# Kernel tuning notes

Measured on AMD Instinct MI355X. Metric: run time of the kernel, lower is better.

Reference implementation:

```python
import jax, jax.numpy as jnp
import numpy as np

K = 16  # neighbors, incl. self


def setup_inputs() -> dict:
    key = jax.random.key(0)
    ks = jax.random.split(key, 16)
    N, C = 8192, 256  # points, channels (inter_channels == in_channels == C)
    s = 0.05
    inp = {
        'coords': jax.random.uniform(ks[0], (N, 3), dtype=jnp.float32) * 100.0,
        'feats': jax.random.normal(ks[1], (N, C), dtype=jnp.float32),
        'theta_w': jax.random.normal(ks[2], (C, C), dtype=jnp.float32) * s,
        'theta_b': jax.random.normal(ks[3], (C,), dtype=jnp.float32) * s,
        'phi_w': jax.random.normal(ks[4], (C, C), dtype=jnp.float32) * s,
        'phi_b': jax.random.normal(ks[5], (C,), dtype=jnp.float32) * s,
        'g_w': jax.random.normal(ks[6], (C, C), dtype=jnp.float32) * s,
        'g_b': jax.random.normal(ks[7], (C,), dtype=jnp.float32) * s,
        'pe1_w1': jax.random.normal(ks[8], (3, C), dtype=jnp.float32) * s,
        'pe1_b1': jax.random.normal(ks[9], (C,), dtype=jnp.float32) * s,
        'pe1_w2': jax.random.normal(ks[10], (C, C), dtype=jnp.float32) * s,
        'pe1_b2': jax.random.normal(ks[11], (C,), dtype=jnp.float32) * s,
        'W_w': jax.random.normal(ks[12], (C, C), dtype=jnp.float32) * s,
        'W_b': jax.random.normal(ks[13], (C,), dtype=jnp.float32) * s,
    }
    return inp


def reference(coords, feats, theta_w, theta_b, phi_w, phi_b, g_w, g_b,
              pe1_w1, pe1_b1, pe1_w2, pe1_b2, W_w, W_b):
    C = feats.shape[-1]
    # KNN (squared dists, includes self as nearest) == pytorch3d knn_points
    sq = jnp.sum(coords * coords, axis=-1)  # [N]
    d2 = sq[:, None] + sq[None, :] - 2.0 * (coords @ coords.T)  # [N,N]
    _, idx = jax.lax.top_k(-d2, K)  # [N,K] sorted by ascending distance

    nn_coords = coords[idx]            # [N,K,3] knn gather
    nn_feats = feats[idx]              # [N,K,C]

    theta_f = feats @ theta_w + theta_b          # [N,C]
    phi_f = nn_feats @ phi_w + phi_b             # [N,K,C]

    delta_coords = nn_coords - coords[:, None, :]  # [N,K,3]
    # pe1 MLP; NOTE: original code uses pe1 for both pe1 and pe2 (shared)
    pe = jax.nn.relu(delta_coords @ pe1_w1 + pe1_b1) @ pe1_w2 + pe1_b2  # [N,K,C]

    delta_features = (pe * (theta_f[:, None, :] - phi_f) + pe) / jnp.sqrt(jnp.float32(C))
    sim = jax.nn.softmax(delta_features, axis=1)  # softmax over K neighbors

    g_feats = nn_feats @ g_w + g_b               # [N,K,C]
    y = jnp.sum(sim * g_feats, axis=1)           # [N,C]

    # W (1x1 Minkowski conv == per-point linear) + residual
    return y @ W_w + W_b + feats
```

## Files before the change

kernel.cpp:

```cpp
#include <hip/hip_runtime.h>

typedef __bf16 bf16_t;
typedef bf16_t bf16x8 __attribute__((ext_vector_type(8)));
typedef bf16_t bf16x4 __attribute__((ext_vector_type(4)));
typedef bf16_t bf16x2 __attribute__((ext_vector_type(2)));
typedef float f32x4 __attribute__((ext_vector_type(4)));
typedef unsigned long long u64;

#define N_PTS 8192
#define C_DIM 256
#define K_NN 16

#define GRID_G    16
#define GRID_NC   (GRID_G * GRID_G * GRID_G)
#define GRID_CELL 6.25f
#define GRID_INV  0.16f

#define CAST_NBLK 2048
#define PREPW_NBLK 320
__global__ __launch_bounds__(256) void prep_kernel(
    const float* __restrict__ feats, bf16_t* __restrict__ fb,
    const float* __restrict__ w0, const float* __restrict__ w1,
    const float* __restrict__ w2, const float* __restrict__ w3,
    const float* __restrict__ w4, bf16_t* __restrict__ wt_base,
    int* __restrict__ cellCount, int* __restrict__ gcount) {
    const int b = blockIdx.x;
    const int t = threadIdx.x;

    if (b < CAST_NBLK) {
        int i = (b * 256 + t) * 4;
        float4 v = *(const float4*)(feats + i);
        bf16x4 o;
        o[0] = (bf16_t)v.x; o[1] = (bf16_t)v.y; o[2] = (bf16_t)v.z; o[3] = (bf16_t)v.w;
        *(bf16x4*)(fb + i) = o;
    } else if (b < CAST_NBLK + PREPW_NBLK) {
        int pb = b - CAST_NBLK;
        int m = pb >> 6;
        int bx = pb & 63;
        const float* src = (m == 0) ? w0 : (m == 1) ? w1 : (m == 2) ? w2 : (m == 3) ? w3 : w4;
        bf16_t* dst = wt_base + m * (C_DIM * C_DIM);
#pragma unroll
        for (int i = 0; i < 4; ++i) {
            int o = bx * 1024 + i * 256 + t;
            int tkb = o >> 9;
            int rem = o & 511;
            int lm = rem >> 5;
            int r = rem & 31;
            int k = (tkb & 7) * 32 + r;
            int n = (tkb >> 3) * 16 + lm;
            dst[o] = (bf16_t)src[k * C_DIM + n];
        }
    } else {
        int zb = b - CAST_NBLK - PREPW_NBLK;
        cellCount[zb * 256 + t] = 0;
        if (zb == 0 && t == 0) *gcount = 0;
    }
}

__global__ __launch_bounds__(256) void grid_count_kernel(const float* __restrict__ coords,
                                                         int* __restrict__ cellCount,
                                                         int* __restrict__ cid) {
    int i = blockIdx.x * 256 + threadIdx.x;
    float x = coords[3 * i + 0], y = coords[3 * i + 1], z = coords[3 * i + 2];
    int cx = (int)(x * GRID_INV); if (cx > GRID_G - 1) cx = GRID_G - 1;
    int cy = (int)(y * GRID_INV); if (cy > GRID_G - 1) cy = GRID_G - 1;
    int cz = (int)(z * GRID_INV); if (cz > GRID_G - 1) cz = GRID_G - 1;
    int c = (cx * GRID_G + cy) * GRID_G + cz;
    cid[i] = c;
    atomicAdd(&cellCount[c], 1);
}

__global__ __launch_bounds__(256) void grid_scan_kernel(const int* __restrict__ cellCount,
                                                        int* __restrict__ cellStart,
                                                        int* __restrict__ cellPtr) {
    __shared__ int part[256];
    int t = threadIdx.x;
    int base = t * 16;
    int v[16];
    int sum = 0;
#pragma unroll
    for (int i = 0; i < 16; ++i) { v[i] = cellCount[base + i]; sum += v[i]; }
    part[t] = sum;
    __syncthreads();
    for (int off = 1; off < 256; off <<= 1) {
        int x = (t >= off) ? part[t - off] : 0;
        __syncthreads();
        part[t] += x;
        __syncthreads();
    }
    int acc = part[t] - sum;
#pragma unroll
    for (int i = 0; i < 16; ++i) {
        cellStart[base + i] = acc;
        cellPtr[base + i] = acc;
        acc += v[i];
    }
    if (t == 255) cellStart[GRID_NC] = acc;
}

__global__ __launch_bounds__(256) void grid_scatter_kernel(
    const float* __restrict__ coords, const int* __restrict__ cid, int* __restrict__ cellPtr,
    float4* __restrict__ sp4, int* __restrict__ sidx) {
    int i = blockIdx.x * 256 + threadIdx.x;
    int c = cid[i];
    int pos = atomicAdd(&cellPtr[c], 1);
    float x = coords[3 * i + 0], y = coords[3 * i + 1], z = coords[3 * i + 2];
    float sq = __fadd_rn(__fadd_rn(__fmul_rn(x, x), __fmul_rn(y, y)), __fmul_rn(z, z));
    sp4[pos] = make_float4(x, y, z, sq);
    sidx[pos] = i;
}

__global__ __launch_bounds__(256) void knn_grid_kernel(
    const float* __restrict__ coords, const int* __restrict__ cellStart,
    const float4* __restrict__ sp4, const int* __restrict__ sidx,
    int* __restrict__ idx_out, int* __restrict__ glist, int* __restrict__ gcount) {
    const int tid = threadIdx.x;
    const int wave = tid >> 6, lane = tid & 63;
    const int q = blockIdx.x * 4 + wave;

    __shared__ int segBase[4][25];
    __shared__ int segPref[4][26];

    const float qx = coords[3 * q + 0], qy = coords[3 * q + 1], qz = coords[3 * q + 2];
    const float sqi = __fadd_rn(__fadd_rn(__fmul_rn(qx, qx), __fmul_rn(qy, qy)),
                                __fmul_rn(qz, qz));

    int cx = (int)(qx * GRID_INV); if (cx > GRID_G - 1) cx = GRID_G - 1;
    int cy = (int)(qy * GRID_INV); if (cy > GRID_G - 1) cy = GRID_G - 1;
    int cz = (int)(qz * GRID_INV); if (cz > GRID_G - 1) cz = GRID_G - 1;
    int wx0 = cx - 2; if (wx0 < 0) wx0 = 0;
    int wx1 = cx + 2; if (wx1 > GRID_G - 1) wx1 = GRID_G - 1;
    int wy0 = cy - 2; if (wy0 < 0) wy0 = 0;
    int wy1 = cy + 2; if (wy1 > GRID_G - 1) wy1 = GRID_G - 1;
    int wz0 = cz - 2; if (wz0 < 0) wz0 = 0;
    int wz1 = cz + 2; if (wz1 > GRID_G - 1) wz1 = GRID_G - 1;

    const float INF = __int_as_float(0x7f800000);
    float rc = INF;
    if (wx0 > 0)          rc = fminf(rc, qx - (float)wx0 * GRID_CELL);
    if (wx1 < GRID_G - 1) rc = fminf(rc, (float)(wx1 + 1) * GRID_CELL - qx);
    if (wy0 > 0)          rc = fminf(rc, qy - (float)wy0 * GRID_CELL);
    if (wy1 < GRID_G - 1) rc = fminf(rc, (float)(wy1 + 1) * GRID_CELL - qy);
    if (wz0 > 0)          rc = fminf(rc, qz - (float)wz0 * GRID_CELL);
    if (wz1 < GRID_G - 1) rc = fminf(rc, (float)(wz1 + 1) * GRID_CELL - qz);
    float rc2 = rc * rc * 0.9999f;

    int nx = wx1 - wx0 + 1, nyc = wy1 - wy0 + 1;
    int ns = nx * nyc;
    if (lane < ns) {
        int scx = wx0 + lane / nyc;
        int scy = wy0 + lane % nyc;
        int b = (scx * GRID_G + scy) * GRID_G;
        int s0 = cellStart[b + wz0];
        int s1 = cellStart[b + wz1 + 1];
        segBase[wave][lane] = s0;
        segPref[wave][lane] = s1 - s0;
    }
    __syncthreads();
    if (lane == 0) {
        int acc = 0;
        for (int s = 0; s < ns; ++s) { int l = segPref[wave][s]; segPref[wave][s] = acc; acc += l; }
        segPref[wave][ns] = acc;
    }
    __syncthreads();

    const int M = segPref[wave][ns];
    bool flag = (M < K_NN) || (M > 320);

    u64 k0 = ~0ull, k1 = ~0ull, k2 = ~0ull, k3 = ~0ull, k4 = ~0ull;
    {
        int s = 0;
#pragma unroll
        for (int slot = 0; slot < 5; ++slot) {
            int t = lane + slot * 64;
            if (t < M) {
                while (t >= segPref[wave][s + 1]) ++s;
                int pos = segBase[wave][s] + (t - segPref[wave][s]);
                float4 v = sp4[pos];
                float dot = __fmaf_rn(v.z, qz, __fmaf_rn(v.y, qy, __fmul_rn(v.x, qx)));
                float d2 = __fsub_rn(__fadd_rn(sqi, v.w), __fmul_rn(2.0f, dot));
                unsigned u = __float_as_uint(d2);
                u = (u & 0x80000000u) ? ~u : (u | 0x80000000u);
                u64 key = (((u64)u) << 32) | (unsigned)sidx[pos];
                if (slot == 0) k0 = key;
                else if (slot == 1) k1 = key;
                else if (slot == 2) k2 = key;
                else if (slot == 3) k3 = key;
                else k4 = key;
            }
        }
    }

    u64 lm2 = k0; int li = 0;
    if (k1 < lm2) { lm2 = k1; li = 1; }
    if (k2 < lm2) { lm2 = k2; li = 2; }
    if (k3 < lm2) { lm2 = k3; li = 3; }
    if (k4 < lm2) { lm2 = k4; li = 4; }
    int keep = 0;
    u64 last = ~0ull;
#pragma unroll 1
    for (int r = 0; r < 16; ++r) {
        u64 w = lm2;
#pragma unroll
        for (int off = 1; off < 64; off <<= 1) {
            u64 o = __shfl_xor(w, off);
            w = (o < w) ? o : w;
        }
        if (lane == r) keep = (int)(unsigned)(w & 0xffffffffull);
        last = w;
        if (lm2 == w) {
            if (li == 0) k0 = ~0ull;
            else if (li == 1) k1 = ~0ull;
            else if (li == 2) k2 = ~0ull;
            else if (li == 3) k3 = ~0ull;
            else k4 = ~0ull;
            lm2 = k0; li = 0;
            if (k1 < lm2) { lm2 = k1; li = 1; }
            if (k2 < lm2) { lm2 = k2; li = 2; }
            if (k3 < lm2) { lm2 = k3; li = 3; }
            if (k4 < lm2) { lm2 = k4; li = 4; }
        }
    }

    if (!flag) {
        unsigned ou = (unsigned)(last >> 32);
        unsigned db = (ou & 0x80000000u) ? (ou ^ 0x80000000u) : ~ou;
        float d16 = __uint_as_float(db);
        if (d16 >= rc2) flag = true;
    }
    if (flag && lane == 0) {
        int sl = atomicAdd(gcount, 1);
        glist[sl] = q;
    }
    if (lane < 16) idx_out[q * K_NN + lane] = keep;
}

__global__ __launch_bounds__(256) void knn_fallback_kernel(const float* __restrict__ coords,
                                                           const int* __restrict__ glist,
                                                           const int* __restrict__ gcount,
                                                           int* __restrict__ idx_out) {
    const int count = *gcount;
    const int tid = threadIdx.x;
    const int wave = tid >> 6, lane = tid & 63;
    __shared__ float red16[4][16];
    __shared__ u64 cand[4][256];
    __shared__ int cnt[4];
    __shared__ int qids[4];
    const float INF = __int_as_float(0x7f800000);
    const float* cp = coords + tid * 96;

#pragma unroll 1
    for (int n0 = blockIdx.x * 4; n0 < count; n0 += gridDim.x * 4) {
        if (tid < 4) {
            cnt[tid] = 0;
            int slot = n0 + tid;
            qids[tid] = glist[slot < count ? slot : count - 1];
        }
        __syncthreads();

        float qx[4], qy[4], qz[4], sqi[4];
#pragma unroll
        for (int q = 0; q < 4; ++q) {
            int id = qids[q];
            qx[q] = coords[3 * id + 0];
            qy[q] = coords[3 * id + 1];
            qz[q] = coords[3 * id + 2];
            sqi[q] = __fadd_rn(__fadd_rn(__fmul_rn(qx[q], qx[q]), __fmul_rn(qy[q], qy[q])),
                               __fmul_rn(qz[q], qz[q]));
        }

        float lmin[4] = {INF, INF, INF, INF};
#pragma unroll
        for (int c = 0; c < 4; ++c) {
            float buf[24];
#pragma unroll
            for (int v = 0; v < 6; ++v)
                *(float4*)(buf + v * 4) = *(const float4*)(cp + c * 24 + v * 4);
#pragma unroll
            for (int p = 0; p < 8; ++p) {
                float x = buf[3 * p + 0], y = buf[3 * p + 1], z = buf[3 * p + 2];
                float sqj = __fadd_rn(__fadd_rn(__fmul_rn(x, x), __fmul_rn(y, y)),
                                      __fmul_rn(z, z));
#pragma unroll
                for (int q = 0; q < 4; ++q) {
                    float dot = __fmaf_rn(z, qz[q], __fmaf_rn(y, qy[q], __fmul_rn(x, qx[q])));
                    float d2 = __fsub_rn(__fadd_rn(sqi[q], sqj), __fmul_rn(2.0f, dot));
                    lmin[q] = fminf(lmin[q], d2);
                }
            }
        }

#pragma unroll
        for (int q = 0; q < 4; ++q) {
            float g = lmin[q];
            g = fminf(g, __shfl_xor(g, 1));
            g = fminf(g, __shfl_xor(g, 2));
            g = fminf(g, __shfl_xor(g, 4));
            g = fminf(g, __shfl_xor(g, 8));
            if ((lane & 15) == 0) red16[q][wave * 4 + (lane >> 4)] = g;
        }
        __syncthreads();

        float tau[4];
#pragma unroll
        for (int q = 0; q < 4; ++q) {
            float t = red16[q][0];
#pragma unroll
            for (int i = 1; i < 16; ++i) t = fmaxf(t, red16[q][i]);
            tau[q] = t;
        }

#pragma unroll
        for (int c = 0; c < 4; ++c) {
            float buf[24];
#pragma unroll
            for (int v = 0; v < 6; ++v)
                *(float4*)(buf + v * 4) = *(const float4*)(cp + c * 24 + v * 4);
#pragma unroll
            for (int p = 0; p < 8; ++p) {
                float x = buf[3 * p + 0], y = buf[3 * p + 1], z = buf[3 * p + 2];
                float sqj = __fadd_rn(__fadd_rn(__fmul_rn(x, x), __fmul_rn(y, y)),
                                      __fmul_rn(z, z));
                int j = tid * 32 + c * 8 + p;
#pragma unroll
                for (int q = 0; q < 4; ++q) {
                    float dot = __fmaf_rn(z, qz[q], __fmaf_rn(y, qy[q], __fmul_rn(x, qx[q])));
                    float d2 = __fsub_rn(__fadd_rn(sqi[q], sqj), __fmul_rn(2.0f, dot));
                    if (d2 <= tau[q]) {
                        unsigned u = __float_as_uint(d2);
                        u = (u & 0x80000000u) ? ~u : (u | 0x80000000u);
                        int slot = atomicAdd(&cnt[q], 1);
                        if (slot < 256)
                            cand[q][slot] = (((u64)u) << 32) | (unsigned)j;
                    }
                }
            }
        }
        __syncthreads();

        int m = cnt[wave]; if (m > 256) m = 256;
        u64 k0 = ~0ull, k1 = ~0ull, k2 = ~0ull, k3 = ~0ull;
        if (lane < m) k0 = cand[wave][lane];
        if (lane + 64 < m) k1 = cand[wave][lane + 64];
        if (lane + 128 < m) k2 = cand[wave][lane + 128];
        if (lane + 192 < m) k3 = cand[wave][lane + 192];
        u64 lm2 = k0; int li = 0;
        if (k1 < lm2) { lm2 = k1; li = 1; }
        if (k2 < lm2) { lm2 = k2; li = 2; }
        if (k3 < lm2) { lm2 = k3; li = 3; }
        int keep = 0;
#pragma unroll 1
        for (int r = 0; r < 16; ++r) {
            u64 w = lm2;
#pragma unroll
            for (int off = 1; off < 64; off <<= 1) {
                u64 o = __shfl_xor(w, off);
                w = (o < w) ? o : w;
            }
            if (lane == r) keep = (int)(unsigned)(w & 0xffffffffull);
            if (lm2 == w) {
                if (li == 0) k0 = ~0ull;
                else if (li == 1) k1 = ~0ull;
                else if (li == 2) k2 = ~0ull;
                else k3 = ~0ull;
                lm2 = k0; li = 0;
                if (k1 < lm2) { lm2 = k1; li = 1; }
                if (k2 < lm2) { lm2 = k2; li = 2; }
                if (k3 < lm2) { lm2 = k3; li = 3; }
            }
        }
        if (n0 + wave < count && lane < 16)
            idx_out[qids[wave] * K_NN + lane] = keep;
        __syncthreads();
    }
}

__global__ __launch_bounds__(256, 2) void proj_kernel(
    const bf16_t* __restrict__ fb, const bf16_t* __restrict__ wt_base,
    const float* __restrict__ tb, const float* __restrict__ pb, const float* __restrict__ gb,
    float* __restrict__ T, bf16_t* __restrict__ PG) {
    const int sel = blockIdx.y;
    const int half = blockIdx.z;
    const bf16_t* Wt = wt_base + sel * (C_DIM * C_DIM);
    const float* bias = (sel == 0) ? tb : (sel == 1) ? pb : gb;
    const int wave = threadIdx.x >> 6, lane = threadIdx.x & 63;
    const int q = lane >> 4, lm = lane & 15;
    const int m0 = blockIdx.x * 64;

    bf16x8 bfr[2][8];
#pragma unroll
    for (int ti = 0; ti < 2; ++ti)
#pragma unroll
        for (int kb = 0; kb < 8; ++kb)
            bfr[ti][kb] = *(const bf16x8*)(Wt + (((half * 8 + wave * 2 + ti) * 8 + kb) << 9) + lm * 32 + q * 8);

    float bv[2];
#pragma unroll
    for (int ti = 0; ti < 2; ++ti) bv[ti] = bias[(half * 8 + wave * 2 + ti) * 16 + lm];

#pragma unroll
    for (int p = 0; p < 4; ++p) {
        const bf16_t* arow = fb + (m0 + p * 16 + lm) * C_DIM + q * 8;
        f32x4 acc[2];
        acc[0] = (f32x4){0.f, 0.f, 0.f, 0.f};
        acc[1] = (f32x4){0.f, 0.f, 0.f, 0.f};
#pragma unroll
        for (int kb = 0; kb < 8; ++kb) {
            bf16x8 a = *(const bf16x8*)(arow + kb * 32);
            acc[0] = __builtin_amdgcn_mfma_f32_16x16x32_bf16(a, bfr[0][kb], acc[0], 0, 0, 0);
            acc[1] = __builtin_amdgcn_mfma_f32_16x16x32_bf16(a, bfr[1][kb], acc[1], 0, 0, 0);
        }

#pragma unroll
        for (int ti = 0; ti < 2; ++ti) {
            int c = (half * 8 + wave * 2 + ti) * 16 + lm;
#pragma unroll
            for (int r = 0; r < 4; ++r) {
                float v = acc[ti][r] + bv[ti];
                int off = (m0 + p * 16 + q * 4 + r) * C_DIM + c;
                if (sel == 0) T[off] = v;
                else if (sel == 1) PG[2 * off] = (bf16_t)v;
                else PG[2 * off + 1] = (bf16_t)v;
            }
        }
    }
}

#define HPAD 264
#define P_BLK 16
#define HROWS (P_BLK * 16)
__global__ __launch_bounds__(512, 4) void pe2_fused_kernel(
    const float* __restrict__ coords, const int* __restrict__ idx,
    const float* __restrict__ T, const bf16_t* __restrict__ PG,
    const float* __restrict__ w1, const float* __restrict__ b1, const float* __restrict__ b2,
    const bf16_t* __restrict__ Wt2, const bf16_t* __restrict__ Wt3,
    const float* __restrict__ Wb, const float* __restrict__ feats,
    float* __restrict__ out) {
    __shared__ __align__(16) bf16_t hbuf[2][16 * HPAD];
    __shared__ __align__(16) bf16_t yl[16][HPAD];
    __shared__ float dxyz[HROWS][3];
    __shared__ int idxl[HROWS];
    const int tid = threadIdx.x;
    const int p0 = blockIdx.x * P_BLK;
    const int wave = tid >> 6, lane = tid & 63;
    const int q = lane >> 4, lm = lane & 15;

    bf16x8 bfr[2][8];
#pragma unroll
    for (int ti = 0; ti < 2; ++ti)
#pragma unroll
        for (int kb = 0; kb < 8; ++kb)
            bfr[ti][kb] = *(const bf16x8*)(Wt2 + (((wave * 2 + ti) * 8 + kb) << 9) + lm * 32 + q * 8);
    float b2c[2];
#pragma unroll
    for (int ti = 0; ti < 2; ++ti) b2c[ti] = b2[(wave * 2 + ti) * 16 + lm];

    if (tid < HROWS) {
        int n = p0 + (tid >> 4);
        int j = idx[n * K_NN + (tid & 15)];
        idxl[tid] = j;
        dxyz[tid][0] = coords[3 * j + 0] - coords[3 * n + 0];
        dxyz[tid][1] = coords[3 * j + 1] - coords[3 * n + 1];
        dxyz[tid][2] = coords[3 * j + 2] - coords[3 * n + 2];
    }
    __syncthreads();

    const int hc = tid & 255;
    const int rh = (tid >> 8) * 8;
    const float wx = w1[hc], wy = w1[C_DIM + hc], wz = w1[2 * C_DIM + hc], bb = b1[hc];

#pragma unroll
    for (int r = 0; r < 8; ++r) {
        int row = rh + r;
        float pre = dxyz[row][0] * wx + dxyz[row][1] * wy + dxyz[row][2] * wz + bb;
        hbuf[0][row * HPAD + hc] = (bf16_t)fmaxf(pre, 0.0f);
    }
    __syncthreads();

#pragma unroll 1
    for (int lp = 0; lp < P_BLK; ++lp) {
        const int n = p0 + lp;
        const int cur = lp & 1;

        int jr[4];
#pragma unroll
        for (int r = 0; r < 4; ++r) jr[r] = idxl[lp * 16 + q * 4 + r];
        bf16x2 pg[2][4];
        float Tn[2];
#pragma unroll
        for (int ti = 0; ti < 2; ++ti) {
            int c = (wave * 2 + ti) * 16 + lm;
            Tn[ti] = T[n * C_DIM + c];
#pragma unroll
            for (int r = 0; r < 4; ++r)
                pg[ti][r] = *(const bf16x2*)(PG + 2 * (jr[r] * C_DIM + c));
        }

        if (lp + 1 < P_BLK) {
            int rb = (lp + 1) * 16;
#pragma unroll
            for (int r = 0; r < 8; ++r) {
                int row = rh + r;
                float pre = dxyz[rb + row][0] * wx + dxyz[rb + row][1] * wy
                          + dxyz[rb + row][2] * wz + bb;
                hbuf[cur ^ 1][row * HPAD + hc] = (bf16_t)fmaxf(pre, 0.0f);
            }
        }

        const bf16_t* hrow = &hbuf[cur][lm * HPAD + q * 8];
        f32x4 acc[2];
        acc[0] = (f32x4){0.f, 0.f, 0.f, 0.f};
        acc[1] = (f32x4){0.f, 0.f, 0.f, 0.f};
#pragma unroll
        for (int kb = 0; kb < 8; ++kb) {
            bf16x8 a = *(const bf16x8*)(hrow + kb * 32);
            acc[0] = __builtin_amdgcn_mfma_f32_16x16x32_bf16(a, bfr[0][kb], acc[0], 0, 0, 0);
            acc[1] = __builtin_amdgcn_mfma_f32_16x16x32_bf16(a, bfr[1][kb], acc[1], 0, 0, 0);
        }

#pragma unroll
        for (int ti = 0; ti < 2; ++ti) {
            int c = (wave * 2 + ti) * 16 + lm;
            float df[4];
#pragma unroll
            for (int r = 0; r < 4; ++r) {
                float pe = acc[ti][r] + b2c[ti];
                df[r] = (pe * (Tn[ti] - (float)pg[ti][r][0]) + pe) * 0.0625f;
            }
            float mx = fmaxf(fmaxf(df[0], df[1]), fmaxf(df[2], df[3]));
            mx = fmaxf(mx, __shfl_xor(mx, 16));
            mx = fmaxf(mx, __shfl_xor(mx, 32));
            float e[4], s = 0.f;
#pragma unroll
            for (int r = 0; r < 4; ++r) { e[r] = __expf(df[r] - mx); s += e[r]; }
            s += __shfl_xor(s, 16);
            s += __shfl_xor(s, 32);
            float inv = 1.0f / s;
            float y = 0.f;
#pragma unroll
            for (int r = 0; r < 4; ++r) y += e[r] * inv * (float)pg[ti][r][1];
            y += __shfl_xor(y, 16);
            y += __shfl_xor(y, 32);
            if (q == 0) yl[lp][c] = (bf16_t)y;
        }
        __syncthreads();
    }

#pragma unroll
    for (int ti = 0; ti < 2; ++ti)
#pragma unroll
        for (int kb = 0; kb < 8; ++kb)
            bfr[ti][kb] = *(const bf16x8*)(Wt3 + (((wave * 2 + ti) * 8 + kb) << 9) + lm * 32 + q * 8);
    float bw[2];
#pragma unroll
    for (int ti = 0; ti < 2; ++ti) bw[ti] = Wb[(wave * 2 + ti) * 16 + lm];

    f32x4 acc2[2];
    acc2[0] = (f32x4){0.f, 0.f, 0.f, 0.f};
    acc2[1] = (f32x4){0.f, 0.f, 0.f, 0.f};
#pragma unroll
    for (int kb = 0; kb < 8; ++kb) {
        bf16x8 a = *(const bf16x8*)(&yl[lm][kb * 32 + q * 8]);
        acc2[0] = __builtin_amdgcn_mfma_f32_16x16x32_bf16(a, bfr[0][kb], acc2[0], 0, 0, 0);
        acc2[1] = __builtin_amdgcn_mfma_f32_16x16x32_bf16(a, bfr[1][kb], acc2[1], 0, 0, 0);
    }

#pragma unroll
    for (int ti = 0; ti < 2; ++ti) {
        int c = (wave * 2 + ti) * 16 + lm;
#pragma unroll
        for (int r = 0; r < 4; ++r) {
            int off = (p0 + q * 4 + r) * C_DIM + c;
            out[off] = acc2[ti][r] + bw[ti] + feats[off];
        }
    }
}

extern "C" void kernel_launch(void* const* d_in, const int* in_sizes, int n_in,
                              void* d_out, int out_size, void* d_ws, size_t ws_size,
                              hipStream_t stream) {
    const float* coords = (const float*)d_in[0];
    const float* feats  = (const float*)d_in[1];
    const float* theta_w = (const float*)d_in[2];
    const float* theta_b = (const float*)d_in[3];
    const float* phi_w   = (const float*)d_in[4];
    const float* phi_b   = (const float*)d_in[5];
    const float* g_w     = (const float*)d_in[6];
    const float* g_b     = (const float*)d_in[7];
    const float* pe1_w1  = (const float*)d_in[8];
    const float* pe1_b1  = (const float*)d_in[9];
    const float* pe1_w2  = (const float*)d_in[10];
    const float* pe1_b2  = (const float*)d_in[11];
    const float* W_w     = (const float*)d_in[12];
    const float* W_b     = (const float*)d_in[13];
    float* out = (float*)d_out;

    char* w = (char*)d_ws;
    size_t off = 0;
    int* idx = (int*)(w + off);        off += (size_t)N_PTS * K_NN * 4;
    bf16_t* fb = (bf16_t*)(w + off);   off += (size_t)N_PTS * C_DIM * 2;
    bf16_t* wt = (bf16_t*)(w + off);   off += (size_t)5 * C_DIM * C_DIM * 2;
    float* T = (float*)(w + off);      off += (size_t)N_PTS * C_DIM * 4;
    bf16_t* PG = (bf16_t*)(w + off);   off += (size_t)N_PTS * C_DIM * 4;
    float4* sp4 = (float4*)(w + off);  off += (size_t)N_PTS * 16;
    int* sidxp = (int*)(w + off);      off += (size_t)N_PTS * 4;
    int* cid       = (int*)(w + off);  off += (size_t)N_PTS * 4;
    int* cellCount = (int*)(w + off);  off += (size_t)GRID_NC * 4;
    int* cellStart = (int*)(w + off);  off += (size_t)(GRID_NC + 1) * 4;
    int* cellPtr   = (int*)(w + off);  off += (size_t)GRID_NC * 4;
    int* glist = (int*)(w + off);      off += (size_t)N_PTS * 4;
    int* gcount = (int*)(w + off);     off += 256;
    (void)ws_size; (void)in_sizes; (void)n_in; (void)out_size;

    prep_kernel<<<CAST_NBLK + PREPW_NBLK + 16, 256, 0, stream>>>(
        feats, fb, theta_w, phi_w, g_w, pe1_w2, W_w, wt, cellCount, gcount);

    grid_count_kernel<<<N_PTS / 256, 256, 0, stream>>>(coords, cellCount, cid);
    grid_scan_kernel<<<1, 256, 0, stream>>>(cellCount, cellStart, cellPtr);
    grid_scatter_kernel<<<N_PTS / 256, 256, 0, stream>>>(coords, cid, cellPtr, sp4, sidxp);
    knn_grid_kernel<<<N_PTS / 4, 256, 0, stream>>>(coords, cellStart, sp4, sidxp,
                                                   idx, glist, gcount);
    knn_fallback_kernel<<<32, 256, 0, stream>>>(coords, glist, gcount, idx);

    proj_kernel<<<dim3(N_PTS / 64, 3, 2), 256, 0, stream>>>(fb, wt, theta_b, phi_b, g_b, T, PG);
    pe2_fused_kernel<<<N_PTS / P_BLK, 512, 0, stream>>>(coords, idx, T, PG,
                                                        pe1_w1, pe1_b1, pe1_b2,
                                                        wt + 3 * C_DIM * C_DIM,
                                                        wt + 4 * C_DIM * C_DIM,
                                                        W_b, feats, out);
}
```

Measured before the change: 190.3 us.

## Merge KNN search and feature projection into one heterogeneous launch

The grid KNN search and the bf16 MFMA projection (theta/phi/g) are independent, so they are fused into a single kernel whose block index selects either a KNN query block or a projection tile. This removes one launch and lets the latency-bound KNN blocks overlap with the compute-bound projection blocks on the GPU. In exchange, the projection blocks lose their launch_bounds(256,2) occupancy hint and now share register and LDS allocation with the KNN path, which could lower occupancy for both.

```diff
diff --git a/kernel.cpp b/kernel.cpp
--- a/kernel.cpp
+++ b/kernel.cpp
@@ -34,9 +34,9 @@
         o[0] = (bf16_t)v.x; o[1] = (bf16_t)v.y; o[2] = (bf16_t)v.z; o[3] = (bf16_t)v.w;
         *(bf16x4*)(fb + i) = o;
     } else if (b < CAST_NBLK + PREPW_NBLK) {
-        int pb = b - CAST_NBLK;
-        int m = pb >> 6;
-        int bx = pb & 63;
+        int pblk = b - CAST_NBLK;
+        int m = pblk >> 6;
+        int bx = pblk & 63;
         const float* src = (m == 0) ? w0 : (m == 1) ? w1 : (m == 2) ? w2 : (m == 3) ? w3 : w4;
         bf16_t* dst = wt_base + m * (C_DIM * C_DIM);
 #pragma unroll
@@ -110,129 +110,184 @@
     sidx[pos] = i;
 }
 
-__global__ __launch_bounds__(256) void knn_grid_kernel(
+#define KNN_NBLK (N_PTS / 4)
+#define PROJ_NBLK (128 * 3 * 2)
+__global__ __launch_bounds__(256) void knn_proj_kernel(
     const float* __restrict__ coords, const int* __restrict__ cellStart,
     const float4* __restrict__ sp4, const int* __restrict__ sidx,
-    int* __restrict__ idx_out, int* __restrict__ glist, int* __restrict__ gcount) {
+    int* __restrict__ idx_out, int* __restrict__ glist, int* __restrict__ gcount,
+    const bf16_t* __restrict__ fb, const bf16_t* __restrict__ wt_base,
+    const float* __restrict__ tb, const float* __restrict__ phb, const float* __restrict__ gb,
+    float* __restrict__ T, bf16_t* __restrict__ PG) {
     const int tid = threadIdx.x;
     const int wave = tid >> 6, lane = tid & 63;
-    const int q = blockIdx.x * 4 + wave;
 
     __shared__ int segBase[4][25];
     __shared__ int segPref[4][26];
 
-    const float qx = coords[3 * q + 0], qy = coords[3 * q + 1], qz = coords[3 * q + 2];
-    const float sqi = __fadd_rn(__fadd_rn(__fmul_rn(qx, qx), __fmul_rn(qy, qy)),
-                                __fmul_rn(qz, qz));
-
-    int cx = (int)(qx * GRID_INV); if (cx > GRID_G - 1) cx = GRID_G - 1;
-    int cy = (int)(qy * GRID_INV); if (cy > GRID_G - 1) cy = GRID_G - 1;
-    int cz = (int)(qz * GRID_INV); if (cz > GRID_G - 1) cz = GRID_G - 1;
-    int wx0 = cx - 2; if (wx0 < 0) wx0 = 0;
-    int wx1 = cx + 2; if (wx1 > GRID_G - 1) wx1 = GRID_G - 1;
-    int wy0 = cy - 2; if (wy0 < 0) wy0 = 0;
-    int wy1 = cy + 2; if (wy1 > GRID_G - 1) wy1 = GRID_G - 1;
-    int wz0 = cz - 2; if (wz0 < 0) wz0 = 0;
-    int wz1 = cz + 2; if (wz1 > GRID_G - 1) wz1 = GRID_G - 1;
-
-    const float INF = __int_as_float(0x7f800000);
-    float rc = INF;
-    if (wx0 > 0)          rc = fminf(rc, qx - (float)wx0 * GRID_CELL);
-    if (wx1 < GRID_G - 1) rc = fminf(rc, (float)(wx1 + 1) * GRID_CELL - qx);
-    if (wy0 > 0)          rc = fminf(rc, qy - (float)wy0 * GRID_CELL);
-    if (wy1 < GRID_G - 1) rc = fminf(rc, (float)(wy1 + 1) * GRID_CELL - qy);
-    if (wz0 > 0)          rc = fminf(rc, qz - (float)wz0 * GRID_CELL);
-    if (wz1 < GRID_G - 1) rc = fminf(rc, (float)(wz1 + 1) * GRID_CELL - qz);
-    float rc2 = rc * rc * 0.9999f;
-
-    int nx = wx1 - wx0 + 1, nyc = wy1 - wy0 + 1;
-    int ns = nx * nyc;
-    if (lane < ns) {
-        int scx = wx0 + lane / nyc;
-        int scy = wy0 + lane % nyc;
-        int b = (scx * GRID_G + scy) * GRID_G;
-        int s0 = cellStart[b + wz0];
-        int s1 = cellStart[b + wz1 + 1];
-        segBase[wave][lane] = s0;
-        segPref[wave][lane] = s1 - s0;
-    }
-    __syncthreads();
-    if (lane == 0) {
-        int acc = 0;
-        for (int s = 0; s < ns; ++s) { int l = segPref[wave][s]; segPref[wave][s] = acc; acc += l; }
-        segPref[wave][ns] = acc;
-    }
-    __syncthreads();
-
-    const int M = segPref[wave][ns];
-    bool flag = (M < K_NN) || (M > 320);
-
-    u64 k0 = ~0ull, k1 = ~0ull, k2 = ~0ull, k3 = ~0ull, k4 = ~0ull;
-    {
-        int s = 0;
-#pragma unroll
-        for (int slot = 0; slot < 5; ++slot) {
-            int t = lane + slot * 64;
-            if (t < M) {
-                while (t >= segPref[wave][s + 1]) ++s;
-                int pos = segBase[wave][s] + (t - segPref[wave][s]);
-                float4 v = sp4[pos];
-                float dot = __fmaf_rn(v.z, qz, __fmaf_rn(v.y, qy, __fmul_rn(v.x, qx)));
-                float d2 = __fsub_rn(__fadd_rn(sqi, v.w), __fmul_rn(2.0f, dot));
-                unsigned u = __float_as_uint(d2);
-                u = (u & 0x80000000u) ? ~u : (u | 0x80000000u);
-                u64 key = (((u64)u) << 32) | (unsigned)sidx[pos];
-                if (slot == 0) k0 = key;
-                else if (slot == 1) k1 = key;
-                else if (slot == 2) k2 = key;
-                else if (slot == 3) k3 = key;
-                else k4 = key;
-            }
-        }
-    }
-
-    u64 lm2 = k0; int li = 0;
-    if (k1 < lm2) { lm2 = k1; li = 1; }
-    if (k2 < lm2) { lm2 = k2; li = 2; }
-    if (k3 < lm2) { lm2 = k3; li = 3; }
-    if (k4 < lm2) { lm2 = k4; li = 4; }
-    int keep = 0;
-    u64 last = ~0ull;
+    if (blockIdx.x < KNN_NBLK) {
+        const int q = blockIdx.x * 4 + wave;
+
+        const float qx = coords[3 * q + 0], qy = coords[3 * q + 1], qz = coords[3 * q + 2];
+        const float sqi = __fadd_rn(__fadd_rn(__fmul_rn(qx, qx), __fmul_rn(qy, qy)),
+                                    __fmul_rn(qz, qz));
+
+        int cx = (int)(qx * GRID_INV); if (cx > GRID_G - 1) cx = GRID_G - 1;
+        int cy = (int)(qy * GRID_INV); if (cy > GRID_G - 1) cy = GRID_G - 1;
+        int cz = (int)(qz * GRID_INV); if (cz > GRID_G - 1) cz = GRID_G - 1;
+        int wx0 = cx - 2; if (wx0 < 0) wx0 = 0;
+        int wx1 = cx + 2; if (wx1 > GRID_G - 1) wx1 = GRID_G - 1;
+        int wy0 = cy - 2; if (wy0 < 0) wy0 = 0;
+        int wy1 = cy + 2; if (wy1 > GRID_G - 1) wy1 = GRID_G - 1;
+        int wz0 = cz - 2; if (wz0 < 0) wz0 = 0;
+        int wz1 = cz + 2; if (wz1 > GRID_G - 1) wz1 = GRID_G - 1;
+
+        const float INF = __int_as_float(0x7f800000);
+        float rc = INF;
+        if (wx0 > 0)          rc = fminf(rc, qx - (float)wx0 * GRID_CELL);
+        if (wx1 < GRID_G - 1) rc = fminf(rc, (float)(wx1 + 1) * GRID_CELL - qx);
+        if (wy0 > 0)          rc = fminf(rc, qy - (float)wy0 * GRID_CELL);
+        if (wy1 < GRID_G - 1) rc = fminf(rc, (float)(wy1 + 1) * GRID_CELL - qy);
+        if (wz0 > 0)          rc = fminf(rc, qz - (float)wz0 * GRID_CELL);
+        if (wz1 < GRID_G - 1) rc = fminf(rc, (float)(wz1 + 1) * GRID_CELL - qz);
+        float rc2 = rc * rc * 0.9999f;
+
+        int nx = wx1 - wx0 + 1, nyc = wy1 - wy0 + 1;
+        int ns = nx * nyc;
+        if (lane < ns) {
+            int scx = wx0 + lane / nyc;
+            int scy = wy0 + lane % nyc;
+            int b = (scx * GRID_G + scy) * GRID_G;
+            int s0 = cellStart[b + wz0];
+            int s1 = cellStart[b + wz1 + 1];
+            segBase[wave][lane] = s0;
+            segPref[wave][lane] = s1 - s0;
+        }
+        __syncthreads();
+        if (lane == 0) {
+            int acc = 0;
+            for (int s = 0; s < ns; ++s) { int l = segPref[wave][s]; segPref[wave][s] = acc; acc += l; }
+            segPref[wave][ns] = acc;
+        }
+        __syncthreads();
+
+        const int M = segPref[wave][ns];
+        bool flag = (M < K_NN) || (M > 320);
+
+        u64 k0 = ~0ull, k1 = ~0ull, k2 = ~0ull, k3 = ~0ull, k4 = ~0ull;
+        {
+            int s = 0;
+#pragma unroll
+            for (int slot = 0; slot < 5; ++slot) {
+                int t = lane + slot * 64;
+                if (t < M) {
+                    while (t >= segPref[wave][s + 1]) ++s;
+                    int pos = segBase[wave][s] + (t - segPref[wave][s]);
+                    float4 v = sp4[pos];
+                    float dot = __fmaf_rn(v.z, qz, __fmaf_rn(v.y, qy, __fmul_rn(v.x, qx)));
+                    float d2 = __fsub_rn(__fadd_rn(sqi, v.w), __fmul_rn(2.0f, dot));
+                    unsigned u = __float_as_uint(d2);
+                    u = (u & 0x80000000u) ? ~u : (u | 0x80000000u);
+                    u64 key = (((u64)u) << 32) | (unsigned)sidx[pos];
+                    if (slot == 0) k0 = key;
+                    else if (slot == 1) k1 = key;
+                    else if (slot == 2) k2 = key;
+                    else if (slot == 3) k3 = key;
+                    else k4 = key;
+                }
+            }
+        }
+
+        u64 lm2 = k0; int li = 0;
+        if (k1 < lm2) { lm2 = k1; li = 1; }
+        if (k2 < lm2) { lm2 = k2; li = 2; }
+        if (k3 < lm2) { lm2 = k3; li = 3; }
+        if (k4 < lm2) { lm2 = k4; li = 4; }
+        int keep = 0;
+        u64 last = ~0ull;
 #pragma unroll 1
-    for (int r = 0; r < 16; ++r) {
-        u64 w = lm2;
-#pragma unroll
-        for (int off = 1; off < 64; off <<= 1) {
-            u64 o = __shfl_xor(w, off);
-            w = (o < w) ? o : w;
-        }
-        if (lane == r) keep = (int)(unsigned)(w & 0xffffffffull);
-        last = w;
-        if (lm2 == w) {
-            if (li == 0) k0 = ~0ull;
-            else if (li == 1) k1 = ~0ull;
-            else if (li == 2) k2 = ~0ull;
-            else if (li == 3) k3 = ~0ull;
-            else k4 = ~0ull;
-            lm2 = k0; li = 0;
-            if (k1 < lm2) { lm2 = k1; li = 1; }
-            if (k2 < lm2) { lm2 = k2; li = 2; }
-            if (k3 < lm2) { lm2 = k3; li = 3; }
-            if (k4 < lm2) { lm2 = k4; li = 4; }
-        }
-    }
-
-    if (!flag) {
-        unsigned ou = (unsigned)(last >> 32);
-        unsigned db = (ou & 0x80000000u) ? (ou ^ 0x80000000u) : ~ou;
-        float d16 = __uint_as_float(db);
-        if (d16 >= rc2) flag = true;
-    }
-    if (flag && lane == 0) {
-        int sl = atomicAdd(gcount, 1);
-        glist[sl] = q;
-    }
-    if (lane < 16) idx_out[q * K_NN + lane] = keep;
+        for (int r = 0; r < 16; ++r) {
+            u64 w = lm2;
+#pragma unroll
+            for (int off = 1; off < 64; off <<= 1) {
+                u64 o = __shfl_xor(w, off);
+                w = (o < w) ? o : w;
+            }
+            if (lane == r) keep = (int)(unsigned)(w & 0xffffffffull);
+            last = w;
+            if (lm2 == w) {
+                if (li == 0) k0 = ~0ull;
+                else if (li == 1) k1 = ~0ull;
+                else if (li == 2) k2 = ~0ull;
+                else if (li == 3) k3 = ~0ull;
+                else k4 = ~0ull;
+                lm2 = k0; li = 0;
+                if (k1 < lm2) { lm2 = k1; li = 1; }
+                if (k2 < lm2) { lm2 = k2; li = 2; }
+                if (k3 < lm2) { lm2 = k3; li = 3; }
+                if (k4 < lm2) { lm2 = k4; li = 4; }
+            }
+        }
+
+        if (!flag) {
+            unsigned ou = (unsigned)(last >> 32);
+            unsigned db = (ou & 0x80000000u) ? (ou ^ 0x80000000u) : ~ou;
+            float d16 = __uint_as_float(db);
+            if (d16 >= rc2) flag = true;
+        }
+        if (flag && lane == 0) {
+            int sl = atomicAdd(gcount, 1);
+            glist[sl] = q;
+        }
+        if (lane < 16) idx_out[q * K_NN + lane] = keep;
+    } else {
+        int pblk = blockIdx.x - KNN_NBLK;
+        const int m0 = (pblk & 127) * 64;
+        const int sg = pblk >> 7;
+        const int sel = sg % 3;
+        const int half = sg / 3;
+        const bf16_t* Wt = wt_base + sel * (C_DIM * C_DIM);
+        const float* bias = (sel == 0) ? tb : (sel == 1) ? phb : gb;
+        const int q = lane >> 4, lm = lane & 15;
+
+        bf16x8 bfr[2][8];
+#pragma unroll
+        for (int ti = 0; ti < 2; ++ti)
+#pragma unroll
+            for (int kb = 0; kb < 8; ++kb)
+                bfr[ti][kb] = *(const bf16x8*)(Wt + (((half * 8 + wave * 2 + ti) * 8 + kb) << 9) + lm * 32 + q * 8);
+
+        float bv[2];
+#pragma unroll
+        for (int ti = 0; ti < 2; ++ti) bv[ti] = bias[(half * 8 + wave * 2 + ti) * 16 + lm];
+
+#pragma unroll
+        for (int p = 0; p < 4; ++p) {
+            const bf16_t* arow = fb + (m0 + p * 16 + lm) * C_DIM + q * 8;
+            f32x4 acc[2];
+            acc[0] = (f32x4){0.f, 0.f, 0.f, 0.f};
+            acc[1] = (f32x4){0.f, 0.f, 0.f, 0.f};
+#pragma unroll
+            for (int kb = 0; kb < 8; ++kb) {
+                bf16x8 a = *(const bf16x8*)(arow + kb * 32);
+                acc[0] = __builtin_amdgcn_mfma_f32_16x16x32_bf16(a, bfr[0][kb], acc[0], 0, 0, 0);
+                acc[1] = __builtin_amdgcn_mfma_f32_16x16x32_bf16(a, bfr[1][kb], acc[1], 0, 0, 0);
+            }
+
+#pragma unroll
+            for (int ti = 0; ti < 2; ++ti) {
+                int c = (half * 8 + wave * 2 + ti) * 16 + lm;
+#pragma unroll
+                for (int r = 0; r < 4; ++r) {
+                    float v = acc[ti][r] + bv[ti];
+                    int off = (m0 + p * 16 + q * 4 + r) * C_DIM + c;
+                    if (sel == 0) T[off] = v;
+                    else if (sel == 1) PG[2 * off] = (bf16_t)v;
+                    else PG[2 * off + 1] = (bf16_t)v;
+                }
+            }
+        }
+    }
 }
 
 __global__ __launch_bounds__(256) void knn_fallback_kernel(const float* __restrict__ coords,
@@ -372,57 +427,6 @@
         if (n0 + wave < count && lane < 16)
             idx_out[qids[wave] * K_NN + lane] = keep;
         __syncthreads();
-    }
-}
-
-__global__ __launch_bounds__(256, 2) void proj_kernel(
-    const bf16_t* __restrict__ fb, const bf16_t* __restrict__ wt_base,
-    const float* __restrict__ tb, const float* __restrict__ pb, const float* __restrict__ gb,
-    float* __restrict__ T, bf16_t* __restrict__ PG) {
-    const int sel = blockIdx.y;
-    const int half = blockIdx.z;
-    const bf16_t* Wt = wt_base + sel * (C_DIM * C_DIM);
-    const float* bias = (sel == 0) ? tb : (sel == 1) ? pb : gb;
-    const int wave = threadIdx.x >> 6, lane = threadIdx.x & 63;
-    const int q = lane >> 4, lm = lane & 15;
-    const int m0 = blockIdx.x * 64;
-
-    bf16x8 bfr[2][8];
-#pragma unroll
-    for (int ti = 0; ti < 2; ++ti)
-#pragma unroll
-        for (int kb = 0; kb < 8; ++kb)
-            bfr[ti][kb] = *(const bf16x8*)(Wt + (((half * 8 + wave * 2 + ti) * 8 + kb) << 9) + lm * 32 + q * 8);
-
-    float bv[2];
-#pragma unroll
-    for (int ti = 0; ti < 2; ++ti) bv[ti] = bias[(half * 8 + wave * 2 + ti) * 16 + lm];
-
-#pragma unroll
-    for (int p = 0; p < 4; ++p) {
-        const bf16_t* arow = fb + (m0 + p * 16 + lm) * C_DIM + q * 8;
-        f32x4 acc[2];
-        acc[0] = (f32x4){0.f, 0.f, 0.f, 0.f};
-        acc[1] = (f32x4){0.f, 0.f, 0.f, 0.f};
-#pragma unroll
-        for (int kb = 0; kb < 8; ++kb) {
-            bf16x8 a = *(const bf16x8*)(arow + kb * 32);
-            acc[0] = __builtin_amdgcn_mfma_f32_16x16x32_bf16(a, bfr[0][kb], acc[0], 0, 0, 0);
-            acc[1] = __builtin_amdgcn_mfma_f32_16x16x32_bf16(a, bfr[1][kb], acc[1], 0, 0, 0);
-        }
-
-#pragma unroll
-        for (int ti = 0; ti < 2; ++ti) {
-            int c = (half * 8 + wave * 2 + ti) * 16 + lm;
-#pragma unroll
-            for (int r = 0; r < 4; ++r) {
-                float v = acc[ti][r] + bv[ti];
-                int off = (m0 + p * 16 + q * 4 + r) * C_DIM + c;
-                if (sel == 0) T[off] = v;
-                else if (sel == 1) PG[2 * off] = (bf16_t)v;
-                else PG[2 * off + 1] = (bf16_t)v;
-            }
-        }
     }
 }
 
@@ -618,11 +622,13 @@
     grid_count_kernel<<<N_PTS / 256, 256, 0, stream>>>(coords, cellCount, cid);
     grid_scan_kernel<<<1, 256, 0, stream>>>(cellCount, cellStart, cellPtr);
     grid_scatter_kernel<<<N_PTS / 256, 256, 0, stream>>>(coords, cid, cellPtr, sp4, sidxp);
-    knn_grid_kernel<<<N_PTS / 4, 256, 0, stream>>>(coords, cellStart, sp4, sidxp,
-                                                   idx, glist, gcount);
+
+    knn_proj_kernel<<<KNN_NBLK + PROJ_NBLK, 256, 0, stream>>>(
+        coords, cellStart, sp4, sidxp, idx, glist, gcount,
+        fb, wt, theta_b, phi_b, g_b, T, PG);
+
     knn_fallback_kernel<<<32, 256, 0, stream>>>(coords, glist, gcount, idx);
 
-    proj_kernel<<<dim3(N_PTS / 64, 3, 2), 256, 0, stream>>>(fb, wt, theta_b, phi_b, g_b, T, PG);
     pe2_fused_kernel<<<N_PTS / P_BLK, 512, 0, stream>>>(coords, idx, T, PG,
                                                         pe1_w1, pe1_b1, pe1_b2,
                                                         wt + 3 * C_DIM * C_DIM,
```

Result: no change. 187.9 us (-1.3%).
